# Performance work log

Hardware: AMD Instinct MI355X
Metric: run time of the kernel (lower is better)

## Reference

```python
import jax, jax.numpy as jnp
import numpy as np

D_MODEL = 1024
N_HEADS = 16
D_HEAD = D_MODEL // N_HEADS
D_FF = 4096
EPS = 1e-5
NEG = -1e10


def setup_inputs() -> dict:
    key = jax.random.key(0)
    ks = jax.random.split(key, 16)
    s = 0.02
    x = jax.random.normal(ks[0], (4, 1024, D_MODEL), dtype=jnp.float32)
    mask = jnp.ones((4, 1, 1, 1024), dtype=jnp.int32)
    return {
        "x": x,
        "mask": mask,
        "Wq": jax.random.normal(ks[1], (D_MODEL, D_MODEL), jnp.float32) * s,
        "Wk": jax.random.normal(ks[2], (D_MODEL, D_MODEL), jnp.float32) * s,
        "Wv": jax.random.normal(ks[3], (D_MODEL, D_MODEL), jnp.float32) * s,
        "Wp": jax.random.normal(ks[4], (D_MODEL, D_MODEL), jnp.float32) * s,
        "bp": jnp.zeros((D_MODEL,), jnp.float32),
        "W1": jax.random.normal(ks[5], (D_MODEL, D_FF), jnp.float32) * s,
        "b1": jnp.zeros((D_FF,), jnp.float32),
        "W2": jax.random.normal(ks[6], (D_FF, D_MODEL), jnp.float32) * s,
        "b2": jnp.zeros((D_MODEL,), jnp.float32),
        "g1": jnp.ones((D_MODEL,), jnp.float32),
        "be1": jnp.zeros((D_MODEL,), jnp.float32),
        "g2": jnp.ones((D_MODEL,), jnp.float32),
        "be2": jnp.zeros((D_MODEL,), jnp.float32),
    }


def _layer_norm(x, g, b):
    mu = jnp.mean(x, axis=-1, keepdims=True)
    var = jnp.mean(jnp.square(x - mu), axis=-1, keepdims=True)
    return (x - mu) * jax.lax.rsqrt(var + EPS) * g + b


def _mha(x, mask, Wq, Wk, Wv, Wp, bp):
    B, L, _ = x.shape
    q = (x @ Wq).reshape(B, L, N_HEADS, D_HEAD).transpose(0, 2, 1, 3)  # (B,H,L,dh)
    k = (x @ Wk).reshape(B, L, N_HEADS, D_HEAD).transpose(0, 2, 1, 3)
    v = (x @ Wv).reshape(B, L, N_HEADS, D_HEAD).transpose(0, 2, 1, 3)
    scores = jnp.einsum('bhqd,bhkd->bhqk', q, k) / jnp.sqrt(jnp.float32(D_HEAD))
    scores = jnp.where(mask == 0, NEG, scores)
    attn = jax.nn.softmax(scores, axis=-1)
    heads = jnp.einsum('bhqk,bhkd->bhqd', attn, v)  # (B,H,L,dh)
    heads = heads.transpose(0, 2, 1, 3).reshape(B, L, D_MODEL)
    return heads @ Wp + bp


def reference(x, mask, Wq, Wk, Wv, Wp, bp, W1, b1, W2, b2, g1, be1, g2, be2):
    # Post-norm residual sublayers (dropout inactive at inference)
    attn_out = _mha(x, mask, Wq, Wk, Wv, Wp, bp)
    h = _layer_norm(x + attn_out, g1, be1)
    ff = jax.nn.relu(h @ W1 + b1) @ W2 + b2
    out = _layer_norm(h + ff, g2, be2)
    return out
```

## Files before the change

### kernel.cpp

```cpp
#include <hip/hip_runtime.h>
#include <hip/hip_bf16.h>

typedef __attribute__((ext_vector_type(8))) short short8;
typedef __attribute__((ext_vector_type(4))) short short4v;
typedef __attribute__((ext_vector_type(4))) float float4v;

static __device__ __forceinline__ float b2f(short s) {
    return __builtin_bit_cast(float, ((unsigned)(unsigned short)s) << 16);
}
static __device__ __forceinline__ short f2b(float f) {
    unsigned x = __builtin_bit_cast(unsigned, f);
    unsigned r = (x + 0x7fffu + ((x >> 16) & 1u)) >> 16;
    return (short)r;
}
static __device__ __forceinline__ void gload_lds16(const short* g, short* l) {
    __builtin_amdgcn_global_load_lds(
        (const __attribute__((address_space(1))) void*)g,
        (__attribute__((address_space(3))) void*)l, 16, 0, 0);
}

__global__ __launch_bounds__(256) void cvt_k(const float* __restrict__ in,
                                             short* __restrict__ out)
{
    const size_t i = ((size_t)blockIdx.x * 256 + threadIdx.x) * 4;
    const float4v v = *(const float4v*)&in[i];
    short4v s;
#pragma unroll
    for (int j = 0; j < 4; j++) s[j] = f2b(v[j]);
    *(short4v*)&out[i] = s;
}

__global__ __launch_bounds__(256) void transpose_cvt_k(const float* __restrict__ in,
                                                       short* __restrict__ out,
                                                       int R, int C)
{
    __shared__ float tile[64][65];
    const int tx = threadIdx.x;
    const int r0 = blockIdx.y * 64, c0 = blockIdx.x * 64;
    const int lr = tx >> 4, lc = (tx & 15) * 4;
#pragma unroll
    for (int p = 0; p < 4; p++) {
        const float4v v = *(const float4v*)&in[(size_t)(r0 + lr + p * 16) * C + c0 + lc];
#pragma unroll
        for (int j = 0; j < 4; j++) tile[lr + p * 16][lc + j] = v[j];
    }
    __syncthreads();
    const int oc = tx >> 3, orr = (tx & 7) * 8;
#pragma unroll
    for (int p = 0; p < 2; p++) {
        const int c = oc + p * 32;
        short8 pk;
#pragma unroll
        for (int j = 0; j < 8; j++) pk[j] = f2b(tile[orr + j][c]);
        *(short8*)&out[(size_t)(c0 + c) * R + r0 + orr] = pk;
    }
}

template<int MODE, int BM, int BN, int KH>
__global__ __launch_bounds__(256) void gemm_bt(const short* __restrict__ X,
                                               const short* __restrict__ Wt,
                                               short* __restrict__ out,
                                               const float* __restrict__ bias,
                                               const short* __restrict__ res,
                                               int M, int N, int K)
{
    constexpr int MI = BM / 32, NI = BN / 32;
    __shared__ short As[KH][BM * 32];
    __shared__ short Bs[KH][BN * 32];
    const int tid = threadIdx.x;
    const int wave = tid >> 6, lane = tid & 63;
    const int quad = lane >> 4, l16 = lane & 15;

    int bx = blockIdx.x, by = blockIdx.y;
    {
        const int nbx = gridDim.x, nby = gridDim.y;
        if ((nby & 7) == 0) {
            const int g = by * nbx + bx;
            const int xcd = g & 7, local = g >> 3, Y = nby >> 3;
            by = xcd * Y + (local % Y);
            bx = local / Y;
        }
    }
    const int m0 = by * BM, n0 = bx * BN;
    const int wm = (wave >> 1) * (BM / 2), wn = (wave & 1) * (BN / 2);

    const int srow = tid >> 2, sc8 = (tid & 3) * 8;

    float4v acc[MI][NI] = {};

    for (int k0 = 0; k0 < K; k0 += KH * 32) {
#pragma unroll
        for (int c = 0; c < BM / 64; c++)
#pragma unroll
            for (int h = 0; h < KH; h++)
                gload_lds16(X + (size_t)(m0 + c * 64 + srow) * K + k0 + h * 32 + sc8,
                            &As[h][(c * 256 + tid) * 8]);
#pragma unroll
        for (int c = 0; c < BN / 64; c++)
#pragma unroll
            for (int h = 0; h < KH; h++)
                gload_lds16(Wt + (size_t)(n0 + c * 64 + srow) * K + k0 + h * 32 + sc8,
                            &Bs[h][(c * 256 + tid) * 8]);
        __syncthreads();
#pragma unroll
        for (int h = 0; h < KH; h++) {
            short8 af[MI], bf[NI];
#pragma unroll
            for (int i = 0; i < MI; i++) af[i] = *(const short8*)&As[h][(wm + i * 16 + l16) * 32 + quad * 8];
#pragma unroll
            for (int i = 0; i < NI; i++) bf[i] = *(const short8*)&Bs[h][(wn + i * 16 + l16) * 32 + quad * 8];
#pragma unroll
            for (int mi = 0; mi < MI; mi++)
#pragma unroll
                for (int ni = 0; ni < NI; ni++)
                    acc[mi][ni] = __builtin_amdgcn_mfma_f32_16x16x32_bf16(af[mi], bf[ni], acc[mi][ni], 0, 0, 0);
        }
        __syncthreads();
    }

#pragma unroll
    for (int mi = 0; mi < MI; mi++) {
#pragma unroll
        for (int ni = 0; ni < NI; ni++) {
            const int gn = n0 + wn + ni * 16 + l16;
            const float bv = (MODE == 2 || MODE == 3) ? bias[gn] : 0.0f;
#pragma unroll
            for (int r = 0; r < 4; r++) {
                const int gm = m0 + wm + mi * 16 + quad * 4 + r;
                float v = acc[mi][ni][r];
                if (MODE == 4) {
                    const int s = gn >> 10;
                    const int n = gn & 1023;
                    const int hh = n >> 6, d = n & 63;
                    const size_t bh16 = (size_t)((gm >> 10) * 16 + hh) << 16;
                    const size_t base = (size_t)s << 22;
                    if (s == 0)      out[base + bh16 + ((size_t)(gm & 1023) << 6) + d] = f2b(v * 0.125f);
                    else if (s == 1) out[base + bh16 + ((size_t)(gm & 1023) << 6) + d] = f2b(v);
                    else             out[base + bh16 + ((size_t)d << 10) + (gm & 1023)] = f2b(v);
                } else if (MODE == 2) {
                    v += bv;
                    v = fmaxf(v, 0.0f);
                    out[(size_t)gm * N + gn] = f2b(v);
                } else {
                    v += bv + b2f(res[(size_t)gm * N + gn]);
                    out[(size_t)gm * N + gn] = f2b(v);
                }
            }
        }
    }
}

__global__ __launch_bounds__(256) void attn_k(const short* __restrict__ Qb,
                                              const short* __restrict__ Kb,
                                              const short* __restrict__ Vt,
                                              const int* __restrict__ mask,
                                              short* __restrict__ heads)
{
    __shared__ short Kl[2][64 * 32];
    __shared__ short Vl[2][64 * 32];
    __shared__ short P[4][16 * 72];
    const int bh = blockIdx.x, qb = blockIdx.y;
    const int b = bh >> 4, h = bh & 15;
    const int tid = threadIdx.x, wave = tid >> 6, lane = tid & 63;
    const int quad = lane >> 4, l16 = lane & 15;
    const int qbase = qb * 64 + wave * 16;
    const short* Qp = Qb + ((size_t)bh << 16) + (size_t)qbase * 64;
    const short* Kp = Kb + ((size_t)bh << 16);
    const short* Vp = Vt + ((size_t)bh << 16);
    const int* mp = mask + (b << 10);

    const short8 bq0 = *(const short8*)&Qp[l16 * 64 + quad * 8];
    const short8 bq1 = *(const short8*)&Qp[l16 * 64 + 32 + quad * 8];

    float rs = 0.0f;
    float4v o[4] = {};
    short* myP = &P[wave][0];

    const int srow = tid >> 2, sc8 = (tid & 3) * 8;

    for (int kc = 0; kc < 1024; kc += 64) {
        gload_lds16(Kp + (size_t)(kc + srow) * 64 + sc8,      &Kl[0][tid * 8]);
        gload_lds16(Kp + (size_t)(kc + srow) * 64 + 32 + sc8, &Kl[1][tid * 8]);
        gload_lds16(Vp + (size_t)srow * 1024 + kc + sc8,      &Vl[0][tid * 8]);
        gload_lds16(Vp + (size_t)srow * 1024 + kc + 32 + sc8, &Vl[1][tid * 8]);
        __syncthreads();

        float4v s[4];
#pragma unroll
        for (int kt = 0; kt < 4; kt++) {
            s[kt] = (float4v){};
            const short8 ka = *(const short8*)&Kl[0][(kt * 16 + l16) * 32 + quad * 8];
            s[kt] = __builtin_amdgcn_mfma_f32_16x16x32_bf16(ka, bq0, s[kt], 0, 0, 0);
            const short8 kb = *(const short8*)&Kl[1][(kt * 16 + l16) * 32 + quad * 8];
            s[kt] = __builtin_amdgcn_mfma_f32_16x16x32_bf16(kb, bq1, s[kt], 0, 0, 0);
        }
#pragma unroll
        for (int kt = 0; kt < 4; kt++) {
            const int4 mv = *(const int4*)&mp[kc + kt * 16 + quad * 4];
            float p0 = mv.x ? __expf(fminf(s[kt][0], 30.f)) : 0.f;
            float p1 = mv.y ? __expf(fminf(s[kt][1], 30.f)) : 0.f;
            float p2 = mv.z ? __expf(fminf(s[kt][2], 30.f)) : 0.f;
            float p3 = mv.w ? __expf(fminf(s[kt][3], 30.f)) : 0.f;
            rs += (p0 + p1) + (p2 + p3);
            short4v w;
            w[0] = f2b(p0); w[1] = f2b(p1); w[2] = f2b(p2); w[3] = f2b(p3);
            *(short4v*)&myP[l16 * 72 + kt * 16 + quad * 4] = w;
        }
        const short8 bp0 = *(const short8*)&myP[l16 * 72 + quad * 8];
        const short8 bp1 = *(const short8*)&myP[l16 * 72 + 32 + quad * 8];
#pragma unroll
        for (int dt = 0; dt < 4; dt++) {
            const short8 va = *(const short8*)&Vl[0][(dt * 16 + l16) * 32 + quad * 8];
            o[dt] = __builtin_amdgcn_mfma_f32_16x16x32_bf16(va, bp0, o[dt], 0, 0, 0);
            const short8 vb = *(const short8*)&Vl[1][(dt * 16 + l16) * 32 + quad * 8];
            o[dt] = __builtin_amdgcn_mfma_f32_16x16x32_bf16(vb, bp1, o[dt], 0, 0, 0);
        }
        __syncthreads();
    }

    rs += __shfl_xor(rs, 16);
    rs += __shfl_xor(rs, 32);
    const float inv = 1.0f / fmaxf(rs, 1e-20f);
    const int gq = qbase + l16;
#pragma unroll
    for (int dt = 0; dt < 4; dt++) {
        short4v w;
#pragma unroll
        for (int r = 0; r < 4; r++) w[r] = f2b(o[dt][r] * inv);
        *(short4v*)&heads[((size_t)(b * 1024 + gq) << 10) + h * 64 + dt * 16 + quad * 4] = w;
    }
}

template<bool F32OUT>
__global__ __launch_bounds__(256) void ln_k(const short* __restrict__ in,
                                            const float* __restrict__ g,
                                            const float* __restrict__ be,
                                            short* __restrict__ outb,
                                            float* __restrict__ outf)
{
    __shared__ float red[8];
    const int row = blockIdx.x, tid = threadIdx.x;
    const short* p = in + ((size_t)row << 10);
    float v[4];
#pragma unroll
    for (int i = 0; i < 4; i++) v[i] = b2f(p[tid + i * 256]);
    float s = v[0] + v[1] + v[2] + v[3];
#pragma unroll
    for (int off = 32; off; off >>= 1) s += __shfl_xor(s, off);
    if ((tid & 63) == 0) red[tid >> 6] = s;
    __syncthreads();
    const float mu = (red[0] + red[1] + red[2] + red[3]) * (1.0f / 1024.0f);
    float vs = 0.f;
#pragma unroll
    for (int i = 0; i < 4; i++) { const float d = v[i] - mu; vs += d * d; }
#pragma unroll
    for (int off = 32; off; off >>= 1) vs += __shfl_xor(vs, off);
    if ((tid & 63) == 0) red[4 + (tid >> 6)] = vs;
    __syncthreads();
    const float rstd = rsqrtf((red[4] + red[5] + red[6] + red[7]) * (1.0f / 1024.0f) + 1e-5f);
#pragma unroll
    for (int i = 0; i < 4; i++) {
        const int c = tid + i * 256;
        const float r = (v[i] - mu) * rstd * g[c] + be[c];
        if (F32OUT) outf[((size_t)row << 10) + c] = r;
        else        outb[((size_t)row << 10) + c] = f2b(r);
    }
}

extern "C" void kernel_launch(void* const* d_in, const int* in_sizes, int n_in,
                              void* d_out, int out_size, void* d_ws, size_t ws_size,
                              hipStream_t stream)
{
    const float* x   = (const float*)d_in[0];
    const int*   mk  = (const int*)d_in[1];
    const float* Wq  = (const float*)d_in[2];
    const float* Wk  = (const float*)d_in[3];
    const float* Wv  = (const float*)d_in[4];
    const float* Wp  = (const float*)d_in[5];
    const float* bp  = (const float*)d_in[6];
    const float* W1  = (const float*)d_in[7];
    const float* b1  = (const float*)d_in[8];
    const float* W2  = (const float*)d_in[9];
    const float* b2  = (const float*)d_in[10];
    const float* g1  = (const float*)d_in[11];
    const float* be1 = (const float*)d_in[12];
    const float* g2  = (const float*)d_in[13];
    const float* be2 = (const float*)d_in[14];
    float* out = (float*)d_out;

    char* ws = (char*)d_ws;
    const size_t MB = (size_t)1 << 20;
    short* xb     = (short*)(ws + 0 * MB);
    short* WqkvT  = (short*)(ws + 8 * MB);
    short* WpT    = (short*)(ws + 14 * MB);
    short* W1T    = (short*)(ws + 16 * MB);
    short* W2T    = (short*)(ws + 24 * MB);
    short* Qb     = (short*)(ws + 32 * MB);
    short* Kb     = (short*)(ws + 40 * MB);
    short* Vt     = (short*)(ws + 48 * MB);
    short* hd     = (short*)(ws + 56 * MB);
    short* u      = (short*)(ws + 32 * MB);
    short* hpre   = (short*)(ws + 64 * MB);
    short* hbuf   = (short*)(ws + 72 * MB);

    const dim3 blk(256);

    cvt_k<<<dim3(4096), blk, 0, stream>>>(x, xb);

    transpose_cvt_k<<<dim3(16, 16), blk, 0, stream>>>(Wq, WqkvT, 1024, 1024);
    transpose_cvt_k<<<dim3(16, 16), blk, 0, stream>>>(Wk, WqkvT + (1 << 20), 1024, 1024);
    transpose_cvt_k<<<dim3(16, 16), blk, 0, stream>>>(Wv, WqkvT + (2 << 20), 1024, 1024);
    transpose_cvt_k<<<dim3(16, 16), blk, 0, stream>>>(Wp, WpT, 1024, 1024);
    transpose_cvt_k<<<dim3(64, 16), blk, 0, stream>>>(W1, W1T, 1024, 4096);
    transpose_cvt_k<<<dim3(16, 64), blk, 0, stream>>>(W2, W2T, 4096, 1024);

    gemm_bt<4, 128, 128, 2><<<dim3(24, 32), blk, 0, stream>>>(xb, WqkvT, Qb, nullptr, nullptr, 4096, 3072, 1024);

    attn_k<<<dim3(64, 16), blk, 0, stream>>>(Qb, Kb, Vt, mk, hd);

    gemm_bt<3, 64, 64, 4><<<dim3(16, 64), blk, 0, stream>>>(hd, WpT, hpre, bp, xb, 4096, 1024, 1024);

    ln_k<false><<<dim3(4096), blk, 0, stream>>>(hpre, g1, be1, hbuf, nullptr);

    gemm_bt<2, 128, 128, 2><<<dim3(32, 32), blk, 0, stream>>>(hbuf, W1T, u, b1, nullptr, 4096, 4096, 1024);

    gemm_bt<3, 64, 64, 4><<<dim3(16, 64), blk, 0, stream>>>(u, W2T, hpre, b2, hbuf, 4096, 1024, 4096);

    ln_k<true><<<dim3(4096), blk, 0, stream>>>(hpre, g2, be2, nullptr, out);
}
```

Before: 358.8 us.

## Use split-K with larger tiles for the FFN down-projection GEMM

The second FFN GEMM switches from 64x64 tiles to 128x128 tiles and splits K into two halves across blockIdx.z. Each half writes a bf16 partial, and a new elementwise kernel sums the partials with bias and residual. This aims for better operand reuse per tile while keeping enough blocks to fill the GPU. The cost is an extra kernel, extra partial-buffer traffic, and rounding the partial sums to bf16.

```diff
diff --git a/kernel.cpp b/kernel.cpp
--- a/kernel.cpp
+++ b/kernel.cpp
@@ -84,11 +84,19 @@
     const int m0 = by * BM, n0 = bx * BN;
     const int wm = (wave >> 1) * (BM / 2), wn = (wave & 1) * (BN / 2);
 
+    int kb = 0, ke = K;
+    short* op = out;
+    if (MODE == 5) {
+        kb = blockIdx.z * (K >> 1);
+        ke = kb + (K >> 1);
+        op = out + (size_t)blockIdx.z * M * N;
+    }
+
     const int srow = tid >> 2, sc8 = (tid & 3) * 8;
 
     float4v acc[MI][NI] = {};
 
-    for (int k0 = 0; k0 < K; k0 += KH * 32) {
+    for (int k0 = kb; k0 < ke; k0 += KH * 32) {
 #pragma unroll
         for (int c = 0; c < BM / 64; c++)
 #pragma unroll
@@ -141,6 +149,8 @@
                     v += bv;
                     v = fmaxf(v, 0.0f);
                     out[(size_t)gm * N + gn] = f2b(v);
+                } else if (MODE == 5) {
+                    op[(size_t)gm * N + gn] = f2b(v);
                 } else {
                     v += bv + b2f(res[(size_t)gm * N + gn]);
                     out[(size_t)gm * N + gn] = f2b(v);
@@ -148,6 +158,23 @@
             }
         }
     }
+}
+
+__global__ __launch_bounds__(256) void sk_red_k(const short* __restrict__ p0,
+                                                const short* __restrict__ p1,
+                                                const float* __restrict__ bias,
+                                                const short* __restrict__ res,
+                                                short* __restrict__ out)
+{
+    const size_t i = ((size_t)blockIdx.x * 256 + threadIdx.x) * 4;
+    const short4v a = *(const short4v*)&p0[i];
+    const short4v b = *(const short4v*)&p1[i];
+    const short4v c = *(const short4v*)&res[i];
+    const float4v bv = *(const float4v*)&bias[i & 1023];
+    short4v w;
+#pragma unroll
+    for (int j = 0; j < 4; j++) w[j] = f2b(b2f(a[j]) + b2f(b[j]) + bv[j] + b2f(c[j]));
+    *(short4v*)&out[i] = w;
 }
 
 __global__ __launch_bounds__(256) void attn_k(const short* __restrict__ Qb,
@@ -302,6 +329,7 @@
     short* u      = (short*)(ws + 32 * MB);
     short* hpre   = (short*)(ws + 64 * MB);
     short* hbuf   = (short*)(ws + 72 * MB);
+    short* part   = (short*)(ws + 0 * MB);
 
     const dim3 blk(256);
 
@@ -324,7 +352,9 @@
 
     gemm_bt<2, 128, 128, 2><<<dim3(32, 32), blk, 0, stream>>>(hbuf, W1T, u, b1, nullptr, 4096, 4096, 1024);
 
-    gemm_bt<3, 64, 64, 4><<<dim3(16, 64), blk, 0, stream>>>(u, W2T, hpre, b2, hbuf, 4096, 1024, 4096);
+    gemm_bt<5, 128, 128, 2><<<dim3(8, 32, 2), blk, 0, stream>>>(u, W2T, part, nullptr, nullptr, 4096, 1024, 4096);
+
+    sk_red_k<<<dim3(4096), blk, 0, stream>>>(part, part + (4u << 20), b2, hbuf, hpre);
 
     ln_k<true><<<dim3(4096), blk, 0, stream>>>(hpre, g2, be2, nullptr, out);
 }
```

Result: faster. 346.1 us (-3.5%).
